# Optimization experiments

Measured on AMD Instinct MI355X. Metric: run time of the kernel, lower is better.

The kernel has to match this reference:

```python
import jax, jax.numpy as jnp
import numpy as np

N = 50000      # nodes
E = 800000     # edges (before self-loops)
IN = 512       # input_dim
ENC = 256      # encoding_dim
HID = 32       # hidden_dim per head
HEADS = 4
OUT = 40       # output_dim (classes)
SLOPE = 0.2    # PyG GATConv negative_slope default


def setup_inputs() -> dict:
    key = jax.random.key(0)
    ks = jax.random.split(key, 14)
    w = lambda k, shape: jax.random.normal(k, shape, jnp.float32) * 0.02
    return {
        "x": jax.random.normal(ks[0], (N, IN), jnp.float32),
        "edge_index": jax.random.randint(ks[1], (2, E), 0, N, jnp.int64),
        # Autoencoder (fc3 unused in its forward)
        "ae_w1": w(ks[2], (IN, ENC)), "ae_b1": jnp.zeros((ENC,), jnp.float32),
        "ae_w2": w(ks[3], (ENC, ENC)), "ae_b2": jnp.zeros((ENC,), jnp.float32),
        # GAT layer 1: ENC -> HID per head, HEADS heads, concat
        "gat1_w": w(ks[4], (ENC, HEADS * HID)),
        "gat1_att_src": w(ks[5], (HEADS, HID)),
        "gat1_att_dst": w(ks[6], (HEADS, HID)),
        "gat1_b": jnp.zeros((HEADS * HID,), jnp.float32),
        # GAT layer 2: HEADS*HID -> OUT, 1 head, no concat (mean)
        "gat2_w": w(ks[7], (HEADS * HID, OUT)),
        "gat2_att_src": w(ks[8], (1, OUT)),
        "gat2_att_dst": w(ks[9], (1, OUT)),
        "gat2_b": jnp.zeros((OUT,), jnp.float32),
        # Residual dense branches
        "res1_w": w(ks[10], (ENC, HEADS * HID)), "res1_b": jnp.zeros((HEADS * HID,), jnp.float32),
        "res2_w": w(ks[11], (HEADS * HID, OUT)), "res2_b": jnp.zeros((OUT,), jnp.float32),
    }


def _gat_conv(x, W, att_src, att_dst, bias, src, dst, heads, ch, concat):
    # x: [N, F_in] -> h: [N, heads, ch]
    h = (x @ W).reshape(-1, heads, ch)
    a_src = jnp.sum(h * att_src, axis=-1)   # [N, heads]
    a_dst = jnp.sum(h * att_dst, axis=-1)   # [N, heads]
    e = jax.nn.leaky_relu(a_src[src] + a_dst[dst], SLOPE)  # [E, heads]
    # segment softmax over edges grouped by target node
    m = jax.ops.segment_max(e, dst, num_segments=N)        # [N, heads]
    ee = jnp.exp(e - m[dst])
    den = jax.ops.segment_sum(ee, dst, num_segments=N)
    alpha = ee / jnp.maximum(den[dst], 1e-16)              # [E, heads]
    out = jax.ops.segment_sum(h[src] * alpha[..., None], dst, num_segments=N)  # [N, heads, ch]
    out = out.reshape(-1, heads * ch) if concat else out.mean(axis=1)
    return out + bias


def reference(x, edge_index, ae_w1, ae_b1, ae_w2, ae_b2,
              gat1_w, gat1_att_src, gat1_att_dst, gat1_b,
              gat2_w, gat2_att_src, gat2_att_dst, gat2_b,
              res1_w, res1_b, res2_w, res2_b):
    # add self-loops (PyG GATConv default)
    loops = jnp.arange(N, dtype=edge_index.dtype)
    src = jnp.concatenate([edge_index[0], loops])
    dst = jnp.concatenate([edge_index[1], loops])

    # autoencoder encode (fc1, fc2 only)
    xe = jax.nn.relu(jax.nn.relu(x @ ae_w1 + ae_b1) @ ae_w2 + ae_b2)

    g1 = _gat_conv(xe, gat1_w, gat1_att_src, gat1_att_dst, gat1_b, src, dst, HEADS, HID, True)
    h = jax.nn.relu(g1 + xe @ res1_w + res1_b)

    g2 = _gat_conv(h, gat2_w, gat2_att_src, gat2_att_dst, gat2_b, src, dst, 1, OUT, False)
    return g2 + h @ res2_w + res2_b
```

## Files before the change

### kernel.cpp

```cpp
#include <hip/hip_runtime.h>
#include <hip/hip_bf16.h>
#include <math.h>

#define HEADS 4
#define OUTC 40
#define SLOPE 0.2f
#define DCAP 128

typedef __attribute__((ext_vector_type(8))) short bf16x8;
typedef __attribute__((ext_vector_type(4))) float f32x4;

__device__ __forceinline__ short f2bf(float f) {
    unsigned u = __float_as_uint(f);
    unsigned r = (u + 0x7FFFu + ((u >> 16) & 1u)) >> 16;
    return (short)r;
}
__device__ __forceinline__ float bf2f(short s) {
    return __uint_as_float(((unsigned)(unsigned short)s) << 16);
}
__device__ __forceinline__ float bfu2f(unsigned short s) {
    return __uint_as_float(((unsigned)s) << 16);
}

typedef const __attribute__((address_space(1))) unsigned int gu32;
typedef __attribute__((address_space(3))) unsigned int lu32;
__device__ __forceinline__ void gll16(const void* src, void* lds) {
    __builtin_amdgcn_global_load_lds((gu32*)src, (lu32*)lds, 16, 0, 0);
}

template<int BM_, int AMODE, int EPI, int FUSE>
__global__ __launch_bounds__(256) void gemm2(
    const float* __restrict__ Af,
    const short* __restrict__ A,
    const short* __restrict__ B,
    const float* __restrict__ bias,
    unsigned short* __restrict__ Obf, unsigned short* __restrict__ Ob2,
    float* __restrict__ Of,
    int M, int N, int K,
    const int* __restrict__ fA, const int* __restrict__ fB,
    const int* __restrict__ fC, const int* __restrict__ fD,
    int* __restrict__ fX, int* __restrict__ fY_,
    int fE, int fN, int fy)
{
    if (FUSE == 1 && (int)blockIdx.y >= fy) {
        int e = ((blockIdx.y - fy) * gridDim.x + blockIdx.x) * 256 + threadIdx.x;
        if (e < fE) fY_[e] = atomicAdd(&fX[fA[e]], 1);
        return;
    }
    if (FUSE == 2 && (int)blockIdx.y >= fy) {
        int e = ((blockIdx.y - fy) * gridDim.x + blockIdx.x) * 256 + threadIdx.x;
        if (e < fE) {
            fX[fD[fB[e]] + fC[e]] = fA[e];
        } else if (e < fE + fN) {
            int n = e - fE;
            fX[fD[n + 1] - 1] = n;
        }
        return;
    }

    constexpr int MI = BM_ / 32;
    __shared__ short smem[BM_ * 64 + 8192];
    short* As = smem;
    short* Bs = smem + BM_ * 64;

    const int tid = threadIdx.x;
    const int wid = tid >> 6, lane = tid & 63;
    const int bm = blockIdx.y * BM_, bn = blockIdx.x * 128;
    const int wm = wid >> 1, wn = wid & 1;
    const int rA = lane & 15, kb = lane >> 4;

    f32x4 acc[MI][4];
    #pragma unroll
    for (int i = 0; i < MI; i++)
        #pragma unroll
        for (int j = 0; j < 4; j++)
            acc[i][j] = (f32x4){0.f, 0.f, 0.f, 0.f};

    const int KT = K >> 6;

    const float* asrcF[BM_ / 32];
    #pragma unroll
    for (int it = 0; it < BM_ / 32; it++) {
        int g = it * 256 + tid;
        int row = g >> 3, gr = g & 7;
        int gsrc = gr ^ (row & 7);
        int grow = bm + row; if (grow > M - 1) grow = M - 1;
        asrcF[it] = AMODE ? (Af + (size_t)grow * K + gsrc * 8) : nullptr;
    }

    f32x4 pf0[BM_ / 32], pf1[BM_ / 32];

    auto LOADA = [&](int kt) {
        #pragma unroll
        for (int it = 0; it < BM_ / 32; it++) {
            const float* s = asrcF[it] + ((size_t)kt << 6);
            pf0[it] = *(const f32x4*)s;
            pf1[it] = *(const f32x4*)(s + 4);
        }
    };
    auto STAGE_A_REG = [&]() {
        #pragma unroll
        for (int it = 0; it < BM_ / 32; it++) {
            bf16x8 v;
            v[0] = f2bf(pf0[it][0]); v[1] = f2bf(pf0[it][1]);
            v[2] = f2bf(pf0[it][2]); v[3] = f2bf(pf0[it][3]);
            v[4] = f2bf(pf1[it][0]); v[5] = f2bf(pf1[it][1]);
            v[6] = f2bf(pf1[it][2]); v[7] = f2bf(pf1[it][3]);
            *(bf16x8*)(As + (size_t)(it * 256 + tid) * 8) = v;
        }
    };
    auto STAGE_A_LDS = [&](int kt) {
        const int k0 = kt << 6;
        #pragma unroll
        for (int it = 0; it < BM_ / 32; it++) {
            int g = it * 256 + tid;
            int row = g >> 3, gr = g & 7;
            int gsrc = gr ^ (row & 7);
            int grow = bm + row; if (grow > M - 1) grow = M - 1;
            gll16(A + (size_t)grow * K + k0 + gsrc * 8,
                  As + (it * 256 + wid * 64) * 8);
        }
    };
    auto STAGE_B = [&](int kt) {
        const int k0 = kt << 6;
        #pragma unroll
        for (int it = 0; it < 4; it++) {
            int g = it * 256 + tid;
            int row = g >> 3, gr = g & 7;
            int gsrc = gr ^ (row & 7);
            gll16(B + (size_t)(bn + row) * K + k0 + gsrc * 8,
                  Bs + (it * 256 + wid * 64) * 8);
        }
    };
    auto COMPUTE = [&]() {
        #pragma unroll
        for (int kc = 0; kc < 2; kc++) {
            bf16x8 a[MI], b[4];
            #pragma unroll
            for (int mi = 0; mi < MI; mi++) {
                int r = wm * (BM_ / 2) + mi * 16 + rA;
                int off = r * 64 + (((kc * 4 + kb) ^ (r & 7)) * 8);
                a[mi] = *(const bf16x8*)(As + off);
            }
            #pragma unroll
            for (int ni = 0; ni < 4; ni++) {
                int r = wn * 64 + ni * 16 + rA;
                int off = r * 64 + (((kc * 4 + kb) ^ (r & 7)) * 8);
                b[ni] = *(const bf16x8*)(Bs + off);
            }
            #pragma unroll
            for (int mi = 0; mi < MI; mi++)
                #pragma unroll
                for (int ni = 0; ni < 4; ni++)
                    acc[mi][ni] = __builtin_amdgcn_mfma_f32_16x16x32_bf16(a[mi], b[ni], acc[mi][ni], 0, 0, 0);
        }
    };

    if (AMODE == 1) LOADA(0);
    for (int kt = 0; kt < KT; kt++) {
        if (AMODE == 0) STAGE_A_LDS(kt); else STAGE_A_REG();
        STAGE_B(kt);
        __syncthreads();
        if (AMODE == 1 && kt + 1 < KT) LOADA(kt + 1);
        COMPUTE();
        __syncthreads();
    }

    #pragma unroll
    for (int ni = 0; ni < 4; ni++) {
        int col = bn + wn * 64 + ni * 16 + rA;
        float bv = (EPI == 0) ? bias[col] : 0.f;
        #pragma unroll
        for (int mi = 0; mi < MI; mi++) {
            #pragma unroll
            for (int j = 0; j < 4; j++) {
                int row = bm + wm * (BM_ / 2) + mi * 16 + kb * 4 + j;
                if (row < M) {
                    float v = acc[mi][ni][j];
                    if (EPI == 0) {
                        v = fmaxf(v + bv, 0.f);
                        Obf[(size_t)row * N + col] = (unsigned short)f2bf(v);
                    } else if (EPI == 1) {
                        if (col < 128) Obf[(size_t)row * 128 + col] = (unsigned short)f2bf(v);
                        else           Ob2[(size_t)row * 128 + (col - 128)] = (unsigned short)f2bf(v);
                    } else {
                        if (col < 80) {
                            v += bias[col];
                            Of[(size_t)row * 80 + col] = v;
                            if (col < OUTC)
                                Obf[(size_t)row * OUTC + col] = (unsigned short)f2bf(v);
                        }
                    }
                }
            }
        }
    }
}

__global__ void wprep(const float* __restrict__ ae_w1, const float* __restrict__ ae_w2,
                      const float* __restrict__ g1w, const float* __restrict__ r1w,
                      const float* __restrict__ g2w, const float* __restrict__ r2w,
                      const float* __restrict__ r2b,
                      short* __restrict__ w1T, short* __restrict__ w2T,
                      short* __restrict__ wc1, short* __restrict__ wc2T,
                      float* __restrict__ cb2) {
    int gid = blockIdx.x * blockDim.x + threadIdx.x;
    if (gid < 131072) {
        int n = gid >> 9, k = gid & 511;
        w1T[gid] = f2bf(ae_w1[(size_t)k * 256 + n]);
        return;
    }
    gid -= 131072;
    if (gid < 65536) {
        int n = gid >> 8, k = gid & 255;
        w2T[gid] = f2bf(ae_w2[(size_t)k * 256 + n]);
        return;
    }
    gid -= 65536;
    if (gid < 65536) {
        int n = gid >> 8, k = gid & 255;
        float v = (n < 128) ? g1w[(size_t)k * 128 + n] : r1w[(size_t)k * 128 + (n - 128)];
        wc1[gid] = f2bf(v);
        return;
    }
    gid -= 65536;
    if (gid < 16384) {
        int n = gid >> 7, k = gid & 127;
        float v = 0.f;
        if (n < OUTC)          v = g2w[k * OUTC + n];
        else if (n < 2 * OUTC) v = r2w[k * OUTC + (n - OUTC)];
        wc2T[gid] = f2bf(v);
        return;
    }
    gid -= 16384;
    if (gid < 80) cb2[gid] = (gid < OUTC) ? 0.f : r2b[gid - OUTC];
}

__global__ void scan_part(const int* __restrict__ deg, int N, int* __restrict__ part) {
    __shared__ int s[256];
    int b = blockIdx.x, t = threadIdx.x;
    int i0 = b * 1024 + t * 4;
    int sum = 0;
    #pragma unroll
    for (int j = 0; j < 4; j++) { int i = i0 + j; if (i < N) sum += deg[i] + 1; }
    s[t] = sum; __syncthreads();
    for (int o = 128; o; o >>= 1) { if (t < o) s[t] += s[t + o]; __syncthreads(); }
    if (t == 0) part[b] = s[0];
}

__global__ void scan_base(int* __restrict__ part, int nb, int* __restrict__ offs) {
    int t = threadIdx.x;
    int v = (t < nb) ? part[t] : 0;
    int v0 = v;
    for (int o = 1; o < 64; o <<= 1) {
        int u = __shfl_up(v, o, 64);
        if (t >= o) v += u;
    }
    if (t < nb) part[t] = v - v0;
    if (t == 0) offs[0] = 0;
}

__global__ void scan_final(const int* __restrict__ deg, int N, const int* __restrict__ part,
                           int* __restrict__ offs) {
    __shared__ int s[256];
    int b = blockIdx.x, t = threadIdx.x;
    int i0 = b * 1024 + t * 4;
    int v[4]; int sum = 0;
    #pragma unroll
    for (int j = 0; j < 4; j++) { int i = i0 + j; v[j] = (i < N) ? deg[i] + 1 : 0; sum += v[j]; }
    s[t] = sum; __syncthreads();
    for (int o = 1; o < 256; o <<= 1) {
        int add = (t >= o) ? s[t - o] : 0;
        __syncthreads();
        s[t] += add;
        __syncthreads();
    }
    int excl = s[t] - sum + part[b];
    #pragma unroll
    for (int j = 0; j < 4; j++) {
        int i = i0 + j;
        if (i < N) { offs[i + 1] = excl + v[j]; excl += v[j]; }
    }
}

__global__ void att1(const unsigned short* __restrict__ h1b, const float* __restrict__ atts,
                     const float* __restrict__ attd, float* __restrict__ as1,
                     float* __restrict__ ad1, int N) {
    int idx = blockIdx.x * blockDim.x + threadIdx.x;
    if (idx >= N * HEADS) return;
    int n = idx >> 2, h = idx & 3;
    const unsigned short* row = h1b + (size_t)n * 128 + h * 32;
    float ss = 0.f, dd = 0.f;
    #pragma unroll
    for (int c4 = 0; c4 < 4; c4++) {
        uint4 v = *(const uint4*)(row + c4 * 8);
        float4 ws1 = *(const float4*)(atts + h * 32 + c4 * 8);
        float4 ws2 = *(const float4*)(atts + h * 32 + c4 * 8 + 4);
        float4 wd1 = *(const float4*)(attd + h * 32 + c4 * 8);
        float4 wd2 = *(const float4*)(attd + h * 32 + c4 * 8 + 4);
        float e0 = bfu2f((unsigned short)(v.x & 0xFFFF)), e1 = bfu2f((unsigned short)(v.x >> 16));
        float e2 = bfu2f((unsigned short)(v.y & 0xFFFF)), e3 = bfu2f((unsigned short)(v.y >> 16));
        float e4 = bfu2f((unsigned short)(v.z & 0xFFFF)), e5 = bfu2f((unsigned short)(v.z >> 16));
        float e6 = bfu2f((unsigned short)(v.w & 0xFFFF)), e7 = bfu2f((unsigned short)(v.w >> 16));
        ss += e0*ws1.x + e1*ws1.y + e2*ws1.z + e3*ws1.w + e4*ws2.x + e5*ws2.y + e6*ws2.z + e7*ws2.w;
        dd += e0*wd1.x + e1*wd1.y + e2*wd1.z + e3*wd1.w + e4*wd2.x + e5*wd2.y + e6*wd2.z + e7*wd2.w;
    }
    as1[idx] = ss; ad1[idx] = dd;
}

__global__ void att2(const float* __restrict__ h2r2, const float* __restrict__ atts,
                     const float* __restrict__ attd, float* __restrict__ as2,
                     float* __restrict__ ad2, int N) {
    int n = blockIdx.x * blockDim.x + threadIdx.x;
    if (n >= N) return;
    const float* row = h2r2 + (size_t)n * 80;
    float ss = 0.f, dd = 0.f;
    #pragma unroll
    for (int c = 0; c < OUTC; c += 4) {
        float4 v = *(const float4*)(row + c);
        float4 ws = *(const float4*)(atts + c);
        float4 wd = *(const float4*)(attd + c);
        ss += v.x*ws.x + v.y*ws.y + v.z*ws.z + v.w*ws.w;
        dd += v.x*wd.x + v.y*wd.y + v.z*wd.z + v.w*wd.w;
    }
    as2[n] = ss; ad2[n] = dd;
}

__global__ __launch_bounds__(256) void gat1_fused(const unsigned short* __restrict__ h1b,
                                                  const unsigned short* __restrict__ r1b,
                                                  const float* __restrict__ as1,
                                                  const float* __restrict__ ad1,
                                                  const int* __restrict__ offs,
                                                  const int* __restrict__ csr,
                                                  const float* __restrict__ gb,
                                                  const float* __restrict__ rb,
                                                  unsigned short* __restrict__ hbufb, int N) {
    __shared__ float sc[4][DCAP * 4];
    __shared__ int  scs[4][DCAP];
    int nl = threadIdx.x >> 6;
    int n = blockIdx.x * 4 + nl;
    if (n >= N) return;
    int t = threadIdx.x & 63;
    int h = t >> 4, l = t & 15;
    int beg = offs[n], d = offs[n + 1] - beg;
    float adst = ad1[n * 4 + h];

    float mx = -INFINITY;
    for (int j = l; j < d; j += 16) {
        int s = csr[beg + j];
        float v = as1[s * 4 + h] + adst;
        v = v >= 0.f ? v : SLOPE * v;
        if (j < DCAP) {
            sc[nl][j * 4 + h] = v;
            if (h == 0) scs[nl][j] = s;
        }
        mx = fmaxf(mx, v);
    }
    #pragma unroll
    for (int o = 8; o; o >>= 1) mx = fmaxf(mx, __shfl_xor(mx, o, 16));
    float den = 0.f;
    for (int j = l; j < d; j += 16) {
        float v;
        if (j < DCAP) v = sc[nl][j * 4 + h];
        else {
            int s = csr[beg + j];
            v = as1[s * 4 + h] + adst;
            v = v >= 0.f ? v : SLOPE * v;
        }
        den += __expf(v - mx);
    }
    #pragma unroll
    for (int o = 8; o; o >>= 1) den += __shfl_xor(den, o, 16);
    float iv = 1.f / fmaxf(den, 1e-16f);

    float acc0 = 0.f, acc1 = 0.f;
    for (int j = 0; j < d; j += 8) {
        int cs[8]; float cw[8];
        #pragma unroll
        for (int u = 0; u < 8; u++) {
            int jj = j + u;
            if (jj < d && jj < DCAP) {
                cs[u] = scs[nl][jj];
                cw[u] = __expf(sc[nl][jj * 4 + h] - mx);
            } else if (jj < d) {
                int s = csr[beg + jj];
                cs[u] = s;
                float v = as1[s * 4 + h] + adst;
                v = v >= 0.f ? v : SLOPE * v;
                cw[u] = __expf(v - mx);
            } else { cs[u] = 0; cw[u] = 0.f; }
        }
        #pragma unroll
        for (int u = 0; u < 8; u++) {
            ushort2 hv = *(const ushort2*)(h1b + (size_t)cs[u] * 128 + 2 * t);
            acc0 += cw[u] * bfu2f(hv.x);
            acc1 += cw[u] * bfu2f(hv.y);
        }
    }
    acc0 *= iv; acc1 *= iv;
    ushort2 rv = *(const ushort2*)(r1b + (size_t)n * 128 + 2 * t);
    float2 gv = *(const float2*)(gb + 2 * t);
    float2 bv = *(const float2*)(rb + 2 * t);
    float o0 = fmaxf(acc0 + gv.x + bv.x + bfu2f(rv.x), 0.f);
    float o1 = fmaxf(acc1 + gv.y + bv.y + bfu2f(rv.y), 0.f);
    ushort2 ov = {(unsigned short)f2bf(o0), (unsigned short)f2bf(o1)};
    *(ushort2*)(hbufb + (size_t)n * 128 + 2 * t) = ov;
}

__global__ __launch_bounds__(256) void gat2_fused(const unsigned short* __restrict__ h2b,
                                                  const float* __restrict__ h2r2,
                                                  const float* __restrict__ as2,
                                                  const float* __restrict__ ad2,
                                                  const int* __restrict__ offs,
                                                  const int* __restrict__ csr,
                                                  const float* __restrict__ gb,
                                                  float* __restrict__ out, int N) {
    __shared__ float sc[4][DCAP];
    __shared__ int  scs[4][DCAP];
    int nl = threadIdx.x >> 6;
    int n = blockIdx.x * 4 + nl;
    if (n >= N) return;
    int t = threadIdx.x & 63;
    int beg = offs[n], d = offs[n + 1] - beg;
    float adst = ad2[n];

    float mx = -INFINITY;
    for (int j = t; j < d; j += 64) {
        int s = csr[beg + j];
        float v = as2[s] + adst;
        v = v >= 0.f ? v : SLOPE * v;
        if (j < DCAP) { sc[nl][j] = v; scs[nl][j] = s; }
        mx = fmaxf(mx, v);
    }
    #pragma unroll
    for (int o = 32; o; o >>= 1) mx = fmaxf(mx, __shfl_xor(mx, o, 64));
    float den = 0.f;
    for (int j = t; j < d; j += 64) {
        float v;
        if (j < DCAP) v = sc[nl][j];
        else {
            int s = csr[beg + j];
            v = as2[s] + adst;
            v = v >= 0.f ? v : SLOPE * v;
        }
        den += __expf(v - mx);
    }
    #pragma unroll
    for (int o = 32; o; o >>= 1) den += __shfl_xor(den, o, 64);
    float iv = 1.f / fmaxf(den, 1e-16f);

    float acc0 = 0.f, acc1 = 0.f;
    for (int j = 0; j < d; j += 8) {
        int cs[8]; float cw[8];
        #pragma unroll
        for (int u = 0; u < 8; u++) {
            int jj = j + u;
            if (jj < d && jj < DCAP) {
                cs[u] = scs[nl][jj];
                cw[u] = __expf(sc[nl][jj] - mx);
            } else if (jj < d) {
                int s = csr[beg + jj];
                cs[u] = s;
                float v = as2[s] + adst;
                v = v >= 0.f ? v : SLOPE * v;
                cw[u] = __expf(v - mx);
            } else { cs[u] = 0; cw[u] = 0.f; }
        }
        if (t < 20) {
            #pragma unroll
            for (int u = 0; u < 8; u++) {
                ushort2 hv = *(const ushort2*)(h2b + (size_t)cs[u] * OUTC + 2 * t);
                acc0 += cw[u] * bfu2f(hv.x);
                acc1 += cw[u] * bfu2f(hv.y);
            }
        }
    }
    if (t < 20) {
        float2 rr = *(const float2*)(h2r2 + (size_t)n * 80 + 40 + 2 * t);
        float2 gv = *(const float2*)(gb + 2 * t);
        float2 ov = {acc0 * iv + gv.x + rr.x, acc1 * iv + gv.y + rr.y};
        *(float2*)(out + (size_t)n * OUTC + 2 * t) = ov;
    }
}

extern "C" void kernel_launch(void* const* d_in, const int* in_sizes, int n_in,
                              void* d_out, int out_size, void* d_ws, size_t ws_size,
                              hipStream_t stream) {
    const float* x      = (const float*)d_in[0];
    const int*   ei     = (const int*)d_in[1];
    const float* ae_w1  = (const float*)d_in[2];
    const float* ae_b1  = (const float*)d_in[3];
    const float* ae_w2  = (const float*)d_in[4];
    const float* ae_b2  = (const float*)d_in[5];
    const float* gat1_w = (const float*)d_in[6];
    const float* g1as   = (const float*)d_in[7];
    const float* g1ad   = (const float*)d_in[8];
    const float* g1b    = (const float*)d_in[9];
    const float* gat2_w = (const float*)d_in[10];
    const float* g2as   = (const float*)d_in[11];
    const float* g2ad   = (const float*)d_in[12];
    const float* g2b    = (const float*)d_in[13];
    const float* res1_w = (const float*)d_in[14];
    const float* res1_b = (const float*)d_in[15];
    const float* res2_w = (const float*)d_in[16];
    const float* res2_b = (const float*)d_in[17];
    float* out = (float*)d_out;

    const int Nn = in_sizes[0] / 512;
    const int E  = in_sizes[1] / 2;
    const int Etot = E + Nn;

    const int* srcA = ei;
    const int* dstA = ei + E;

    char* W = (char*)d_ws;
    size_t off = 0;
    auto alloc = [&](size_t bytes) { char* p = W + off; off += (bytes + 255) & ~(size_t)255; return p; };

    unsigned short* y1b   = (unsigned short*)alloc((size_t)Nn * 256 * 2);
    unsigned short* xeb   = (unsigned short*)alloc((size_t)Nn * 256 * 2);
    unsigned short* h1b   = (unsigned short*)alloc((size_t)Nn * 128 * 2);
    unsigned short* r1b   = (unsigned short*)alloc((size_t)Nn * 128 * 2);
    unsigned short* hbufb = (unsigned short*)alloc((size_t)Nn * 128 * 2);
    float*          h2r2  = (float*)alloc((size_t)Nn * 80 * 4);
    unsigned short* h2bf  = (unsigned short*)alloc((size_t)Nn * OUTC * 2);

    short* w1T  = (short*)alloc(256 * 512 * 2);
    short* w2T  = (short*)alloc(256 * 256 * 2);
    short* wc1  = (short*)alloc(256 * 256 * 2);
    short* wc2T = (short*)alloc(128 * 128 * 2);
    float* cb2  = (float*)alloc(80 * 4);
    float* as1  = (float*)alloc((size_t)Nn * HEADS * 4);
    float* ad1  = (float*)alloc((size_t)Nn * HEADS * 4);
    float* as2  = (float*)alloc((size_t)Nn * 4);
    float* ad2  = (float*)alloc((size_t)Nn * 4);
    int* deg  = (int*)alloc((size_t)Nn * 4);
    int* offs = (int*)alloc((size_t)(Nn + 1) * 4);
    int* rank = (int*)alloc((size_t)E * 4);
    int* part = (int*)alloc(256 * 4);
    int* csr  = (int*)alloc((size_t)Etot * 4);

    {
        int total = 131072 + 65536 + 65536 + 16384 + 80;
        wprep<<<(total + 255) / 256, 256, 0, stream>>>(
            ae_w1, ae_w2, gat1_w, res1_w, gat2_w, res2_w, res2_b,
            w1T, w2T, wc1, wc2T, cb2);
    }
    hipMemsetAsync(deg, 0, (size_t)Nn * sizeof(int), stream);

    const int gy1 = (Nn + 31) / 32;
    const int gy2 = (Nn + 63) / 64;
    const int cntRows  = (E + 511) / 512;
    const int scatRows = (E + Nn + 511) / 512;

    gemm2<32, 1, 0, 1><<<dim3(2, gy1 + cntRows), 256, 0, stream>>>(
        x, nullptr, w1T, ae_b1, y1b, nullptr, nullptr, Nn, 256, 512,
        dstA, nullptr, nullptr, nullptr, deg, rank, E, 0, gy1);

    int nb = (Nn + 1023) / 1024;
    scan_part<<<nb, 256, 0, stream>>>(deg, Nn, part);
    scan_base<<<1, 64, 0, stream>>>(part, nb, offs);
    scan_final<<<nb, 256, 0, stream>>>(deg, Nn, part, offs);

    gemm2<64, 0, 0, 2><<<dim3(2, gy2 + scatRows), 256, 0, stream>>>(
        nullptr, (const short*)y1b, w2T, ae_b2, xeb, nullptr, nullptr, Nn, 256, 256,
        srcA, dstA, rank, offs, csr, nullptr, E, Nn, gy2);

    gemm2<64, 0, 1, 0><<<dim3(2, gy2), 256, 0, stream>>>(
        nullptr, (const short*)xeb, wc1, nullptr, h1b, r1b, nullptr, Nn, 256, 256,
        nullptr, nullptr, nullptr, nullptr, nullptr, nullptr, 0, 0, 0);

    att1<<<(Nn * HEADS + 255) / 256, 256, 0, stream>>>(h1b, g1as, g1ad, as1, ad1, Nn);
    gat1_fused<<<(Nn + 3) / 4, 256, 0, stream>>>(h1b, r1b, as1, ad1, offs, csr, g1b, res1_b, hbufb, Nn);

    gemm2<64, 0, 2, 0><<<dim3(1, gy2), 256, 0, stream>>>(
        nullptr, (const short*)hbufb, wc2T, cb2, h2bf, nullptr, h2r2, Nn, 128, 128,
        nullptr, nullptr, nullptr, nullptr, nullptr, nullptr, 0, 0, 0);

    att2<<<(Nn + 255) / 256, 256, 0, stream>>>(h2r2, g2as, g2ad, as2, ad2, Nn);
    gat2_fused<<<(Nn + 3) / 4, 256, 0, stream>>>(h2bf, h2r2, as2, ad2, offs, csr, g2b, out, Nn);
}
```

Baseline: 239.8 us.

## Pre-convert x to bf16 in a fused prep kernel and use LDS-direct GEMM path

Adds a prep kernel that converts the fp32 input x to a bf16 buffer, and folds the weight preparation and the degree zeroing into the same launch, which removes the separate memset. The first GEMM then reads bf16 x through the direct global-to-LDS path with 64-row tiles instead of loading fp32 into registers and converting there. This saves a launch and simplifies the GEMM, but adds a full extra pass over x: reading about 100MB of fp32 and writing 50MB of bf16, which the GEMM then reads back.

```diff
diff --git a/kernel.cpp b/kernel.cpp
--- a/kernel.cpp
+++ b/kernel.cpp
@@ -78,37 +78,6 @@
 
     const int KT = K >> 6;
 
-    const float* asrcF[BM_ / 32];
-    #pragma unroll
-    for (int it = 0; it < BM_ / 32; it++) {
-        int g = it * 256 + tid;
-        int row = g >> 3, gr = g & 7;
-        int gsrc = gr ^ (row & 7);
-        int grow = bm + row; if (grow > M - 1) grow = M - 1;
-        asrcF[it] = AMODE ? (Af + (size_t)grow * K + gsrc * 8) : nullptr;
-    }
-
-    f32x4 pf0[BM_ / 32], pf1[BM_ / 32];
-
-    auto LOADA = [&](int kt) {
-        #pragma unroll
-        for (int it = 0; it < BM_ / 32; it++) {
-            const float* s = asrcF[it] + ((size_t)kt << 6);
-            pf0[it] = *(const f32x4*)s;
-            pf1[it] = *(const f32x4*)(s + 4);
-        }
-    };
-    auto STAGE_A_REG = [&]() {
-        #pragma unroll
-        for (int it = 0; it < BM_ / 32; it++) {
-            bf16x8 v;
-            v[0] = f2bf(pf0[it][0]); v[1] = f2bf(pf0[it][1]);
-            v[2] = f2bf(pf0[it][2]); v[3] = f2bf(pf0[it][3]);
-            v[4] = f2bf(pf1[it][0]); v[5] = f2bf(pf1[it][1]);
-            v[6] = f2bf(pf1[it][2]); v[7] = f2bf(pf1[it][3]);
-            *(bf16x8*)(As + (size_t)(it * 256 + tid) * 8) = v;
-        }
-    };
     auto STAGE_A_LDS = [&](int kt) {
         const int k0 = kt << 6;
         #pragma unroll
@@ -156,12 +125,10 @@
         }
     };
 
-    if (AMODE == 1) LOADA(0);
     for (int kt = 0; kt < KT; kt++) {
-        if (AMODE == 0) STAGE_A_LDS(kt); else STAGE_A_REG();
+        STAGE_A_LDS(kt);
         STAGE_B(kt);
         __syncthreads();
-        if (AMODE == 1 && kt + 1 < KT) LOADA(kt + 1);
         COMPUTE();
         __syncthreads();
     }
@@ -197,43 +164,70 @@
     }
 }
 
-__global__ void wprep(const float* __restrict__ ae_w1, const float* __restrict__ ae_w2,
-                      const float* __restrict__ g1w, const float* __restrict__ r1w,
-                      const float* __restrict__ g2w, const float* __restrict__ r2w,
-                      const float* __restrict__ r2b,
-                      short* __restrict__ w1T, short* __restrict__ w2T,
-                      short* __restrict__ wc1, short* __restrict__ wc2T,
-                      float* __restrict__ cb2) {
-    int gid = blockIdx.x * blockDim.x + threadIdx.x;
-    if (gid < 131072) {
-        int n = gid >> 9, k = gid & 511;
-        w1T[gid] = f2bf(ae_w1[(size_t)k * 256 + n]);
+__global__ void prep(const float* __restrict__ x, unsigned int* __restrict__ xb,
+                     long xtotal,
+                     const float* __restrict__ ae_w1, const float* __restrict__ ae_w2,
+                     const float* __restrict__ g1w, const float* __restrict__ r1w,
+                     const float* __restrict__ g2w, const float* __restrict__ r2w,
+                     const float* __restrict__ r2b,
+                     short* __restrict__ w1T, short* __restrict__ w2T,
+                     short* __restrict__ wc1, short* __restrict__ wc2T,
+                     float* __restrict__ cb2,
+                     int* __restrict__ deg, int Nn,
+                     int xblocks, int wblocks) {
+    int b = blockIdx.x;
+    if (b < xblocks) {
+        long i = ((long)b * 256 + threadIdx.x) * 8;
+        if (i >= xtotal) return;
+        float4 a = *(const float4*)(x + i);
+        float4 c = *(const float4*)(x + i + 4);
+        uint4 o;
+        o.x = (unsigned short)f2bf(a.x) | ((unsigned)(unsigned short)f2bf(a.y) << 16);
+        o.y = (unsigned short)f2bf(a.z) | ((unsigned)(unsigned short)f2bf(a.w) << 16);
+        o.z = (unsigned short)f2bf(c.x) | ((unsigned)(unsigned short)f2bf(c.y) << 16);
+        o.w = (unsigned short)f2bf(c.z) | ((unsigned)(unsigned short)f2bf(c.w) << 16);
+        *(uint4*)(xb + i / 2) = o;
         return;
     }
-    gid -= 131072;
-    if (gid < 65536) {
-        int n = gid >> 8, k = gid & 255;
-        w2T[gid] = f2bf(ae_w2[(size_t)k * 256 + n]);
+    b -= xblocks;
+    if (b < wblocks) {
+        int gid = b * 256 + threadIdx.x;
+        if (gid < 131072) {
+            int n = gid >> 9, k = gid & 511;
+            w1T[gid] = f2bf(ae_w1[(size_t)k * 256 + n]);
+            return;
+        }
+        gid -= 131072;
+        if (gid < 65536) {
+            int n = gid >> 8, k = gid & 255;
+            w2T[gid] = f2bf(ae_w2[(size_t)k * 256 + n]);
+            return;
+        }
+        gid -= 65536;
+        if (gid < 65536) {
+            int n = gid >> 8, k = gid & 255;
+            float v = (n < 128) ? g1w[(size_t)k * 128 + n] : r1w[(size_t)k * 128 + (n - 128)];
+            wc1[gid] = f2bf(v);
+            return;
+        }
+        gid -= 65536;
+        if (gid < 16384) {
+            int n = gid >> 7, k = gid & 127;
+            float v = 0.f;
+            if (n < OUTC)          v = g2w[k * OUTC + n];
+            else if (n < 2 * OUTC) v = r2w[k * OUTC + (n - OUTC)];
+            wc2T[gid] = f2bf(v);
+            return;
+        }
+        gid -= 16384;
+        if (gid < 80) cb2[gid] = (gid < OUTC) ? 0.f : r2b[gid - OUTC];
         return;
     }
-    gid -= 65536;
-    if (gid < 65536) {
-        int n = gid >> 8, k = gid & 255;
-        float v = (n < 128) ? g1w[(size_t)k * 128 + n] : r1w[(size_t)k * 128 + (n - 128)];
-        wc1[gid] = f2bf(v);
-        return;
-    }
-    gid -= 65536;
-    if (gid < 16384) {
-        int n = gid >> 7, k = gid & 127;
-        float v = 0.f;
-        if (n < OUTC)          v = g2w[k * OUTC + n];
-        else if (n < 2 * OUTC) v = r2w[k * OUTC + (n - OUTC)];
-        wc2T[gid] = f2bf(v);
-        return;
-    }
-    gid -= 16384;
-    if (gid < 80) cb2[gid] = (gid < OUTC) ? 0.f : r2b[gid - OUTC];
+    b -= wblocks;
+    {
+        int i = b * 256 + threadIdx.x;
+        if (i < Nn) deg[i] = 0;
+    }
 }
 
 __global__ void scan_part(const int* __restrict__ deg, int N, int* __restrict__ part) {
@@ -517,6 +511,7 @@
     size_t off = 0;
     auto alloc = [&](size_t bytes) { char* p = W + off; off += (bytes + 255) & ~(size_t)255; return p; };
 
+    unsigned short* xb    = (unsigned short*)alloc((size_t)Nn * 512 * 2);
     unsigned short* y1b   = (unsigned short*)alloc((size_t)Nn * 256 * 2);
     unsigned short* xeb   = (unsigned short*)alloc((size_t)Nn * 256 * 2);
     unsigned short* h1b   = (unsigned short*)alloc((size_t)Nn * 128 * 2);
@@ -540,22 +535,23 @@
     int* part = (int*)alloc(256 * 4);
     int* csr  = (int*)alloc((size_t)Etot * 4);
 
-    {
-        int total = 131072 + 65536 + 65536 + 16384 + 80;
-        wprep<<<(total + 255) / 256, 256, 0, stream>>>(
-            ae_w1, ae_w2, gat1_w, res1_w, gat2_w, res2_w, res2_b,
-            w1T, w2T, wc1, wc2T, cb2);
-    }
-    hipMemsetAsync(deg, 0, (size_t)Nn * sizeof(int), stream);
-
-    const int gy1 = (Nn + 31) / 32;
+    long xtotal = (long)Nn * 512;
+    int xblocks = (int)((xtotal / 8 + 255) / 256);
+    int wtotal  = 131072 + 65536 + 65536 + 16384 + 80;
+    int wblocks = (wtotal + 255) / 256;
+    int dblocks = (Nn + 255) / 256;
+    prep<<<xblocks + wblocks + dblocks, 256, 0, stream>>>(
+        x, (unsigned int*)xb, xtotal,
+        ae_w1, ae_w2, gat1_w, res1_w, gat2_w, res2_w, res2_b,
+        w1T, w2T, wc1, wc2T, cb2, deg, Nn, xblocks, wblocks);
+
     const int gy2 = (Nn + 63) / 64;
     const int cntRows  = (E + 511) / 512;
     const int scatRows = (E + Nn + 511) / 512;
 
-    gemm2<32, 1, 0, 1><<<dim3(2, gy1 + cntRows), 256, 0, stream>>>(
-        x, nullptr, w1T, ae_b1, y1b, nullptr, nullptr, Nn, 256, 512,
-        dstA, nullptr, nullptr, nullptr, deg, rank, E, 0, gy1);
+    gemm2<64, 0, 0, 1><<<dim3(2, gy2 + cntRows), 256, 0, stream>>>(
+        nullptr, (const short*)xb, w1T, ae_b1, y1b, nullptr, nullptr, Nn, 256, 512,
+        dstA, nullptr, nullptr, nullptr, deg, rank, E, 0, gy2);
 
     int nb = (Nn + 1023) / 1024;
     scan_part<<<nb, 256, 0, stream>>>(deg, Nn, part);
```

Result: slower. 260.6 us (+8.7%).
